# Kernel tuning notes

Hardware: AMD Instinct MI355X
Metric: run time of the kernel (lower is better)

The kernel has to match this reference:

```python
import jax, jax.numpy as jnp
import numpy as np

B, S, D, H, K = 2, 1024, 1024, 16, 33  # batch, seq, d_model, heads, rel buckets (k+1)
d = D // H


def setup_inputs() -> dict:
    key = jax.random.key(0)
    ks = jax.random.split(key, 16)
    w = lambda k, shape: jax.random.normal(k, shape, dtype=jnp.float32) * 0.02
    return {
        "hidden_state": jax.random.normal(ks[0], (B, S, D), dtype=jnp.float32),
        "pos_indices": jax.random.randint(ks[1], (B, S, S), 0, K),
        "mask": jax.random.bernoulli(ks[2], 0.1, (B, 1, 1, S)),
        "Wq": w(ks[3], (D, D)), "bq": w(ks[4], (D,)),
        "Wk": w(ks[5], (D, D)), "bk": w(ks[6], (D,)),
        "Wv": w(ks[7], (D, D)), "bv": w(ks[8], (D,)),
        "Wo": w(ks[9], (D, D)), "bo": w(ks[10], (D,)),
        "rel_q": w(ks[11], (H, K, d)),
        "rel_k": w(ks[12], (H, K, d)),
        "rel_v": w(ks[13], (H, K, d)),
    }


def reference(hidden_state, pos_indices, mask, Wq, bq, Wk, bk, Wv, bv, Wo, bo,
              rel_q, rel_k, rel_v):
    b, s, dm = hidden_state.shape
    h, k_, dp = rel_q.shape
    # projections -> [B,H,S,d]
    def proj(x, W, bias):
        return (x @ W + bias).reshape(b, s, h, dp).transpose(0, 2, 1, 3)
    q = proj(hidden_state, Wq, bq)
    kk = proj(hidden_state, Wk, bk)
    v = proj(hidden_state, Wv, bv)
    # scale_factor = 1 (c2c) + 1 (rel_q) + 1 (rel_k)
    scale = 1.0 / np.sqrt(dp * 3).astype(np.float32)
    # content-to-content
    c2c = jnp.einsum("bhid,bhjd->bhij", q, kk) * scale
    idx = jnp.broadcast_to(pos_indices[:, None], (b, h, s, s))
    # position-to-content: raw [B,H,K,S], gathered along K with per-(i,j) bucket
    raw_p2c = jnp.einsum("hkd,bhjd->bhkj", rel_q, kk) * scale
    p2c = jnp.take_along_axis(raw_p2c, idx, axis=2)
    # content-to-position: raw [B,H,S,K], gathered along K
    raw_c2p = jnp.einsum("bhid,hkd->bhik", q, rel_k) * scale
    c2p = jnp.take_along_axis(raw_c2p, idx, axis=3)
    scores = c2c + p2c + c2p
    scores = jnp.where(mask, jnp.float32(-1e9), scores)
    probs = jax.nn.softmax(scores, axis=-1)  # dropout is identity in eval
    ctx = jnp.einsum("bhij,bhjd->bhid", probs, v)
    # value-side relative term: sum_j P[i,j] * rel_v[bucket(i,j)]
    oh = jax.nn.one_hot(pos_indices, k_, dtype=probs.dtype)  # [B,S,S,K]
    agg = jnp.einsum("bhij,bijk->bhik", probs, oh)
    ctx = ctx + jnp.einsum("bhik,hkd->bhid", agg, rel_v)
    out = ctx.transpose(0, 2, 1, 3).reshape(b, s, dm)
    return out @ Wo + bo
```

## Files before the change

### kernel.cpp

```cpp
#include <hip/hip_runtime.h>
#include <hip/hip_bf16.h>

#define B_ 2
#define S_ 1024
#define D_ 1024
#define H_ 16
#define K_ 33
#define DH 64
#define SCALE 0.07216878364870322f
#define FXS 32768.0f
#define FXI (1.0f / 32768.0f)

typedef __attribute__((ext_vector_type(8))) short bf16x8;
typedef __attribute__((ext_vector_type(4))) float f32x4;

__device__ __forceinline__ float b2f(unsigned short u) {
    return __uint_as_float(((unsigned int)u) << 16);
}
__device__ __forceinline__ unsigned short f2b(float f) {
    unsigned int u = __float_as_uint(f);
    u += 0x7FFFu + ((u >> 16) & 1u);
    return (unsigned short)(u >> 16);
}
__device__ __forceinline__ float ldf(const void* p, int i, int f32) {
    return f32 ? ((const float*)p)[i] : b2f(((const unsigned short*)p)[i]);
}
__device__ __forceinline__ float4 ldf4(const void* p, int i, int f32) {
    if (f32) return *(const float4*)((const float*)p + i);
    ushort4 u = *(const ushort4*)((const unsigned short*)p + i);
    return make_float4(b2f(u.x), b2f(u.y), b2f(u.z), b2f(u.w));
}
__device__ __forceinline__ float4 ldb4(const unsigned short* p, int i) {
    ushort4 u = *(const ushort4*)(p + i);
    return make_float4(b2f(u.x), b2f(u.y), b2f(u.z), b2f(u.w));
}

__global__ __launch_bounds__(256) void prep(const void* __restrict__ hidden,
                                            const void* __restrict__ mask,
                                            int* __restrict__ flags,
                                            float* __restrict__ mflag) {
    __shared__ int cnt;
    __shared__ int mev[6];
    const int t = threadIdx.x;
    if (t == 0) cnt = 0;
    if (t < 6) mev[t] = 0;
    __syncthreads();
    const unsigned short* hu = (const unsigned short*)hidden;
    int c = 0;
    for (int i = t; i < 2048; i += 256) {
        int e = (hu[i] >> 7) & 0xFF;
        if (e >= 0x8E) c++;
    }
    if (c) atomicAdd(&cnt, c);
    const unsigned char* mb = (const unsigned char*)mask;
    int e_bf = 0, e_f32 = 0, e_f64 = 0, e_f16 = 0, e_u8 = 0;
    for (int p = t; p < 2048; p += 256) {
        unsigned char v = mb[p];
        if ((p & 7) == 6 && v == 0xF0) e_f64 = 1;
        if ((p & 3) == 1 && v == 0x3F) e_bf = 1;
        if ((p & 3) == 3 && v == 0x3F) e_f32 = 1;
        if ((p & 1) == 1 && v == 0x3C) e_f16 = 1;
        if ((p & 3) != 0 && v != 0) e_u8 = 1;
    }
    if (e_f64) atomicOr(&mev[5], 1);
    if (e_bf)  atomicOr(&mev[3], 1);
    if (e_f32) atomicOr(&mev[2], 1);
    if (e_f16) atomicOr(&mev[4], 1);
    if (e_u8)  atomicOr(&mev[1], 1);
    __syncthreads();
    const int f32flag = (cnt >= 8) ? 1 : 0;
    const int mm = mev[5] ? 5 : (mev[3] ? 3 : (mev[2] ? 2 : (mev[4] ? 4 : (mev[1] ? 1 : 0))));
    if (t == 0) { flags[0] = f32flag; flags[2] = mm; }
    for (int j = t; j < B_ * S_; j += 256) {
        int m;
        if (mm == 5)      m = (((const double*)mask)[j] != 0.0);
        else if (mm == 3 || mm == 4) m = (((const unsigned short*)mask)[j] != 0);
        else if (mm == 2) m = (((const float*)mask)[j] != 0.f);
        else if (mm == 1) m = (mb[j] != 0);
        else              m = (((const int*)mask)[j] != 0);
        mflag[j] = m ? 1.f : 0.f;
    }
}

__global__ __launch_bounds__(256) void pos_pack(const int* __restrict__ pos,
                                                unsigned char* __restrict__ pos8) {
    int i = blockIdx.x * 256 + threadIdx.x;
    if (i >= (B_ * S_ * S_) / 4) return;
    int4 p = *(const int4*)&pos[i * 4];
    uchar4 o;
    o.x = (unsigned char)min(max(p.x, 0), K_ - 1);
    o.y = (unsigned char)min(max(p.y, 0), K_ - 1);
    o.z = (unsigned char)min(max(p.z, 0), K_ - 1);
    o.w = (unsigned char)min(max(p.w, 0), K_ - 1);
    *(uchar4*)&pos8[i * 4] = o;
}

__global__ __launch_bounds__(512, 2) void gemm_qkv_mfma(const void* __restrict__ X,
                                                        const void* __restrict__ W0,
                                                        const void* __restrict__ W1,
                                                        const void* __restrict__ W2,
                                                        const void* __restrict__ b0,
                                                        const void* __restrict__ b1,
                                                        const void* __restrict__ b2,
                                                        const int* __restrict__ flags,
                                                        unsigned short* __restrict__ q,
                                                        unsigned short* __restrict__ kk_,
                                                        unsigned short* __restrict__ v) {
    __shared__ unsigned short Asl[128][40];
    __shared__ unsigned short Bsl[128][40];
    const int f32u = flags[0];
    const int z = blockIdx.z;
    const void* W = z == 0 ? W0 : (z == 1 ? W1 : W2);
    const void* bias = z == 0 ? b0 : (z == 1 ? b1 : b2);
    unsigned short* outp = z == 0 ? q : (z == 1 ? kk_ : v);
    const int m0 = blockIdx.y * 128, n0 = blockIdx.x * 128;
    const int t = threadIdx.x;
    const int w = t >> 6, lane = t & 63;
    const int wr = w >> 2, wc = w & 3;
    const int lm = lane & 15, lg = lane >> 4;

    const int am = t >> 2, ac8 = (t & 3) * 8;
    const int bn = t & 127, bkq = (t >> 7) * 8;

    f32x4 acc[4][2] = {};
    float4 pa0, pa1;
    float pbx[8];

    {
        int base = (m0 + am) * 1024 + ac8;
        pa0 = ldf4(X, base, f32u);
        pa1 = ldf4(X, base + 4, f32u);
#pragma unroll
        for (int qi = 0; qi < 8; ++qi)
            pbx[qi] = ldf(W, (bkq + qi) * 1024 + n0 + bn, f32u);
    }

    for (int k0 = 0; k0 < 1024; k0 += 32) {
        {
            ushort4 u0 = {f2b(pa0.x), f2b(pa0.y), f2b(pa0.z), f2b(pa0.w)};
            ushort4 u1 = {f2b(pa1.x), f2b(pa1.y), f2b(pa1.z), f2b(pa1.w)};
            *(ushort4*)&Asl[am][ac8] = u0;
            *(ushort4*)&Asl[am][ac8 + 4] = u1;
#pragma unroll
            for (int qi = 0; qi < 8; qi += 2) {
                unsigned int pk = (unsigned int)f2b(pbx[qi]) |
                                  ((unsigned int)f2b(pbx[qi + 1]) << 16);
                *(unsigned int*)&Bsl[bn][bkq + qi] = pk;
            }
        }
        __syncthreads();
        if (k0 + 32 < 1024) {
            int kn = k0 + 32;
            int base = (m0 + am) * 1024 + kn + ac8;
            pa0 = ldf4(X, base, f32u);
            pa1 = ldf4(X, base + 4, f32u);
#pragma unroll
            for (int qi = 0; qi < 8; ++qi)
                pbx[qi] = ldf(W, (kn + bkq + qi) * 1024 + n0 + bn, f32u);
        }
        bf16x8 af[4], bfr[2];
#pragma unroll
        for (int mi = 0; mi < 4; ++mi)
            af[mi] = *(const bf16x8*)&Asl[wr * 64 + mi * 16 + lm][lg * 8];
#pragma unroll
        for (int nj = 0; nj < 2; ++nj)
            bfr[nj] = *(const bf16x8*)&Bsl[wc * 32 + nj * 16 + lm][lg * 8];
#pragma unroll
        for (int mi = 0; mi < 4; ++mi)
#pragma unroll
            for (int nj = 0; nj < 2; ++nj)
                acc[mi][nj] = __builtin_amdgcn_mfma_f32_16x16x32_bf16(af[mi], bfr[nj],
                                                                      acc[mi][nj], 0, 0, 0);
        __syncthreads();
    }
#pragma unroll
    for (int nj = 0; nj < 2; ++nj) {
        int n = n0 + wc * 32 + nj * 16 + lm;
        float bv = ldf(bias, n, f32u);
        int hh = n >> 6, dd = n & 63;
#pragma unroll
        for (int mi = 0; mi < 4; ++mi) {
#pragma unroll
            for (int r = 0; r < 4; ++r) {
                int m = m0 + wr * 64 + mi * 16 + lg * 4 + r;
                int bb = m >> 10, ii = m & 1023;
                outp[((bb * H_ + hh) * S_ + ii) * DH + dd] = f2b(acc[mi][nj][r] + bv);
            }
        }
    }
}

__global__ __launch_bounds__(512, 2) void gemm_out_mfma(const unsigned short* __restrict__ X,
                                                        const void* __restrict__ W,
                                                        const void* __restrict__ bias,
                                                        const int* __restrict__ flags,
                                                        float* __restrict__ out) {
    __shared__ unsigned short Asl[128][40];
    __shared__ unsigned short Bsl[128][40];
    const int f32u = flags[0];
    const int m0 = blockIdx.y * 128, n0 = blockIdx.x * 128;
    const int t = threadIdx.x;
    const int w = t >> 6, lane = t & 63;
    const int wr = w >> 2, wc = w & 3;
    const int lm = lane & 15, lg = lane >> 4;

    const int am = t >> 2, ac8 = (t & 3) * 8;
    const int bn = t & 127, bkq = (t >> 7) * 8;

    f32x4 acc[4][2] = {};
    ushort4 pa0, pa1;
    float pbx[8];

    {
        const ushort4* src = (const ushort4*)&X[(m0 + am) * 1024 + ac8];
        pa0 = src[0];
        pa1 = src[1];
#pragma unroll
        for (int qi = 0; qi < 8; ++qi)
            pbx[qi] = ldf(W, (bkq + qi) * 1024 + n0 + bn, f32u);
    }

    for (int k0 = 0; k0 < 1024; k0 += 32) {
        {
            *(ushort4*)&Asl[am][ac8] = pa0;
            *(ushort4*)&Asl[am][ac8 + 4] = pa1;
#pragma unroll
            for (int qi = 0; qi < 8; qi += 2) {
                unsigned int pk = (unsigned int)f2b(pbx[qi]) |
                                  ((unsigned int)f2b(pbx[qi + 1]) << 16);
                *(unsigned int*)&Bsl[bn][bkq + qi] = pk;
            }
        }
        __syncthreads();
        if (k0 + 32 < 1024) {
            int kn = k0 + 32;
            const ushort4* src = (const ushort4*)&X[(m0 + am) * 1024 + kn + ac8];
            pa0 = src[0];
            pa1 = src[1];
#pragma unroll
            for (int qi = 0; qi < 8; ++qi)
                pbx[qi] = ldf(W, (kn + bkq + qi) * 1024 + n0 + bn, f32u);
        }
        bf16x8 af[4], bfr[2];
#pragma unroll
        for (int mi = 0; mi < 4; ++mi)
            af[mi] = *(const bf16x8*)&Asl[wr * 64 + mi * 16 + lm][lg * 8];
#pragma unroll
        for (int nj = 0; nj < 2; ++nj)
            bfr[nj] = *(const bf16x8*)&Bsl[wc * 32 + nj * 16 + lm][lg * 8];
#pragma unroll
        for (int mi = 0; mi < 4; ++mi)
#pragma unroll
            for (int nj = 0; nj < 2; ++nj)
                acc[mi][nj] = __builtin_amdgcn_mfma_f32_16x16x32_bf16(af[mi], bfr[nj],
                                                                      acc[mi][nj], 0, 0, 0);
        __syncthreads();
    }
#pragma unroll
    for (int nj = 0; nj < 2; ++nj) {
        int n = n0 + wc * 32 + nj * 16 + lm;
        float bv = ldf(bias, n, f32u);
#pragma unroll
        for (int mi = 0; mi < 4; ++mi) {
#pragma unroll
            for (int r = 0; r < 4; ++r) {
                int m = m0 + wr * 64 + mi * 16 + lg * 4 + r;
                out[m * 1024 + n] = acc[mi][nj][r] + bv;
            }
        }
    }
}

__global__ __launch_bounds__(256) void rel_p2c(const unsigned short* __restrict__ kws,
                                               const void* __restrict__ relq,
                                               const int* __restrict__ flags,
                                               unsigned short* __restrict__ p2c) {
    __shared__ float kt[64][68];
    __shared__ float rq[33][68];
    const int f32u = flags[0];
    const int bh = blockIdx.y, h = bh & 15;
    const int j0 = blockIdx.x * 64;
    const int t = threadIdx.x;
#pragma unroll
    for (int qq = 0; qq < 4; ++qq) {
        int idx = t + 256 * qq;
        int j = idx >> 4, d4 = idx & 15;
        *(float4*)&kt[j][d4 * 4] = ldb4(kws, (bh * S_ + j0 + j) * DH + d4 * 4);
    }
    for (int idx = t; idx < 33 * 16; idx += 256) {
        int k = idx >> 4, d4 = idx & 15;
        *(float4*)&rq[k][d4 * 4] = ldf4(relq, (h * K_ + k) * DH + d4 * 4, f32u);
    }
    __syncthreads();
    for (int o = t; o < 33 * 64; o += 256) {
        int k = o >> 6, j = o & 63;
        float s = 0.f;
#pragma unroll
        for (int d4 = 0; d4 < 16; ++d4) {
            float4 a = *(const float4*)&rq[k][d4 * 4];
            float4 b = *(const float4*)&kt[j][d4 * 4];
            s += a.x * b.x + a.y * b.y + a.z * b.z + a.w * b.w;
        }
        p2c[(bh * K_ + k) * S_ + j0 + j] = f2b(s * SCALE);
    }
}

__global__ __launch_bounds__(256) void rel_c2p(const unsigned short* __restrict__ qws,
                                               const void* __restrict__ relk,
                                               const int* __restrict__ flags,
                                               unsigned short* __restrict__ c2p) {
    __shared__ float qt[64][68];
    __shared__ float rk[33][68];
    const int f32u = flags[0];
    const int bh = blockIdx.y, h = bh & 15;
    const int i0 = blockIdx.x * 64;
    const int t = threadIdx.x;
#pragma unroll
    for (int qq = 0; qq < 4; ++qq) {
        int idx = t + 256 * qq;
        int i = idx >> 4, d4 = idx & 15;
        *(float4*)&qt[i][d4 * 4] = ldb4(qws, (bh * S_ + i0 + i) * DH + d4 * 4);
    }
    for (int idx = t; idx < 33 * 16; idx += 256) {
        int k = idx >> 4, d4 = idx & 15;
        *(float4*)&rk[k][d4 * 4] = ldf4(relk, (h * K_ + k) * DH + d4 * 4, f32u);
    }
    __syncthreads();
    for (int o = t; o < 64 * 33; o += 256) {
        int i = o / 33, k = o % 33;
        float s = 0.f;
#pragma unroll
        for (int d4 = 0; d4 < 16; ++d4) {
            float4 a = *(const float4*)&qt[i][d4 * 4];
            float4 b = *(const float4*)&rk[k][d4 * 4];
            s += a.x * b.x + a.y * b.y + a.z * b.z + a.w * b.w;
        }
        c2p[(bh * S_ + i0 + i) * K_ + k] = f2b(s * SCALE);
    }
}

#define PS_OFF   0
#define VT_OFF   32768
#define P2CS_OFF 32768
#define C2P_OFF  50176
#define AG_OFF   54528
#define RV_OFF   63232
#define MF_OFF   67456
#define ATTN_LDS 68480

__device__ __forceinline__ int ps_addr(int il, int jc) {
    return PS_OFF + il * 512 + ((jc * 2) ^ ((il & 7) << 4));
}

__global__ __launch_bounds__(512, 4) void attn_mfma(const unsigned short* __restrict__ qws,
                                                    const unsigned short* __restrict__ kws,
                                                    const unsigned short* __restrict__ vws,
                                                    const unsigned short* __restrict__ p2c,
                                                    const unsigned short* __restrict__ c2p,
                                                    const float* __restrict__ mflag,
                                                    const unsigned char* __restrict__ pos8,
                                                    const int* __restrict__ pos32,
                                                    int use8,
                                                    const void* __restrict__ relv,
                                                    const int* __restrict__ flags,
                                                    unsigned short* __restrict__ ctxo) {
    extern __shared__ char smem[];
    const int f32u = flags[0];
    const int lin = blockIdx.y * 16 + blockIdx.x;
    const int logi = (lin & 7) * 64 + (lin >> 3);
    const int bh = logi >> 4, b = bh >> 4, h = bh & 15;
    const int i0 = (logi & 15) * 64;
    const int t = threadIdx.x;
    const int w = t >> 6, lane = t & 63;
    const int lm = lane & 15, lg = lane >> 4;
    const int iband = (w & 3) * 16;
    const int jh = w >> 2;
    const int dbase = jh * 32;

    unsigned int* agU = (unsigned int*)(smem + AG_OFF);
    unsigned short* c2pS = (unsigned short*)(smem + C2P_OFF);
    unsigned short* rvS = (unsigned short*)(smem + RV_OFF);
    unsigned char* mfS = (unsigned char*)(smem + MF_OFF);

    for (int idx = t; idx < 64 * 33; idx += 512) {
        int il = idx / 33, k = idx % 33;
        c2pS[il * 34 + k] = c2p[(bh * S_ + i0 + il) * K_ + k];
    }
    for (int idx = t; idx < 33 * 64; idx += 512) {
        int k = idx >> 6, d = idx & 63;
        rvS[k * 64 + d] = f2b(ldf(relv, (h * K_ + k) * DH + d, f32u));
    }
    for (int idx = t; idx < 1024; idx += 512)
        mfS[idx] = (mflag[b * S_ + idx] != 0.f) ? 1 : 0;
    for (int idx = t; idx < 64 * 34; idx += 512) agU[idx] = 0u;

    bf16x8 aq0 = *(const bf16x8*)&qws[(bh * S_ + i0 + iband + lm) * DH + lg * 8];
    bf16x8 aq1 = *(const bf16x8*)&qws[(bh * S_ + i0 + iband + lm) * DH + 32 + lg * 8];
    f32x4 acc0 = {}, acc1 = {};

    const int p2cbase = bh * K_ * S_;
    const int rowbase = (b * S_ + i0 + iband + lg * 4) * S_;
    __syncthreads();

    for (int c = 0; c < 4; ++c) {
        for (int idx = t; idx < 33 * 32; idx += 512) {
            int k = idx >> 5, v8 = idx & 31;
            uint4 src = *(const uint4*)&p2c[p2cbase + k * S_ + c * 256 + v8 * 8];
            unsigned int* dst = (unsigned int*)(smem + P2CS_OFF + k * 516 + v8 * 16);
            dst[0] = src.x; dst[1] = src.y; dst[2] = src.z; dst[3] = src.w;
        }
        __syncthreads();

        for (int jt = 0; jt < 8; ++jt) {
            const int jc = jh * 128 + jt * 16 + lm;
            const int jcol = c * 256 + jc;
            int pb4[4];
            if (use8) {
#pragma unroll
                for (int r = 0; r < 4; ++r)
                    pb4[r] = pos8[rowbase + r * S_ + jcol];
            } else {
#pragma unroll
                for (int r = 0; r < 4; ++r) {
                    int p = pos32[rowbase + r * S_ + jcol];
                    pb4[r] = min(max(p, 0), K_ - 1);
                }
            }
            bf16x8 kf0 = *(const bf16x8*)&kws[(bh * S_ + jcol - lm + lm) * DH + lg * 8];
            bf16x8 kf1 = *(const bf16x8*)&kws[(bh * S_ + jcol - lm + lm) * DH + 32 + lg * 8];
            f32x4 a = {};
            a = __builtin_amdgcn_mfma_f32_16x16x32_bf16(aq0, kf0, a, 0, 0, 0);
            a = __builtin_amdgcn_mfma_f32_16x16x32_bf16(aq1, kf1, a, 0, 0, 0);
            const int masked = mfS[jcol];
#pragma unroll
            for (int r = 0; r < 4; ++r) {
                int il = iband + lg * 4 + r;
                int pb = pb4[r];
                float gv = b2f(*(const unsigned short*)(smem + P2CS_OFF + pb * 516 + jc * 2));
                float s = a[r] * SCALE + gv + b2f(c2pS[il * 34 + pb]);
                float ev = masked ? 0.f : __expf(s);
                *(unsigned short*)(smem + ps_addr(il, jc)) = f2b(ev);
                atomicAdd(&agU[il * 34 + pb], (unsigned int)(ev * FXS + 0.5f));
            }
        }
        __syncthreads();

        for (int st = 0; st < 2; ++st) {
#pragma unroll
            for (int u = 0; u < 2; ++u) {
                int idx = t + u * 512;
                int jj = idx >> 3;
                int a8 = idx & 7;
                int d0 = a8 * 8;
                int j = c * 256 + st * 128 + jj;
                bf16x8 vv = *(const bf16x8*)&vws[(bh * S_ + j) * DH + d0];
#pragma unroll
                for (int e = 0; e < 8; ++e) {
                    int ee = (e + a8) & 7;
                    *(unsigned short*)(smem + VT_OFF + (d0 + ee) * 272 + jj * 2) =
                        ((short*)&vv)[ee];
                }
            }
            __syncthreads();
#pragma unroll
            for (int ks = 0; ks < 4; ++ks) {
                int jcb = st * 128 + ks * 32 + lg * 8;
                bf16x8 af = *(const bf16x8*)(smem + ps_addr(iband + lm, jcb));
                bf16x8 b0 = *(const bf16x8*)(smem + VT_OFF + (dbase + lm) * 272 +
                                             (ks * 32 + lg * 8) * 2);
                bf16x8 b1 = *(const bf16x8*)(smem + VT_OFF + (dbase + 16 + lm) * 272 +
                                             (ks * 32 + lg * 8) * 2);
                acc0 = __builtin_amdgcn_mfma_f32_16x16x32_bf16(af, b0, acc0, 0, 0, 0);
                acc1 = __builtin_amdgcn_mfma_f32_16x16x32_bf16(af, b1, acc1, 0, 0, 0);
            }
            __syncthreads();
        }
    }

#pragma unroll
    for (int r = 0; r < 4; ++r) {
        int il = iband + lg * 4 + r;
        float rs = 0.f;
        float o0 = acc0[r], o1 = acc1[r];
        for (int kb = 0; kb < K_; ++kb) {
            float a = (float)agU[il * 34 + kb] * FXI;
            rs += a;
            o0 += a * b2f(rvS[kb * 64 + dbase + lm]);
            o1 += a * b2f(rvS[kb * 64 + dbase + 16 + lm]);
        }
        float inv = 1.0f / rs;
        ctxo[(b * S_ + i0 + il) * D_ + h * DH + dbase + lm] = f2b(o0 * inv);
        ctxo[(b * S_ + i0 + il) * D_ + h * DH + dbase + 16 + lm] = f2b(o1 * inv);
    }
}

extern "C" void kernel_launch(void* const* d_in, const int* in_sizes, int n_in,
                              void* d_out, int out_size, void* d_ws, size_t ws_size,
                              hipStream_t stream) {
    const void* hidden = d_in[0];
    const void* pos = d_in[1];
    const void* mask = d_in[2];
    const void* Wq = d_in[3];
    const void* bq = d_in[4];
    const void* Wk = d_in[5];
    const void* bk = d_in[6];
    const void* Wv = d_in[7];
    const void* bv = d_in[8];
    const void* Wo = d_in[9];
    const void* bo = d_in[10];
    const void* rq = d_in[11];
    const void* rk = d_in[12];
    const void* rv = d_in[13];

    unsigned char* wsb = (unsigned char*)d_ws;
    size_t o = 0;
    int* flags = (int*)(wsb + o);            o += 256;
    float* mfl = (float*)(wsb + o);          o += 2048 * 4;
    o = (o + 255) & ~(size_t)255;
    unsigned short* qb   = (unsigned short*)(wsb + o); o += 4194304;
    unsigned short* kb   = (unsigned short*)(wsb + o); o += 4194304;
    unsigned short* vb   = (unsigned short*)(wsb + o); o += 4194304;
    unsigned short* p2cb = (unsigned short*)(wsb + o); o += 2162688;
    unsigned short* c2pb = (unsigned short*)(wsb + o); o += 2162688;
    unsigned short* ctxb = (unsigned short*)(wsb + o); o += 4194304;
    unsigned char* pos8  = (unsigned char*)(wsb + o);  o += 2097152;
    const int use8 = (ws_size >= o) ? 1 : 0;

    float* out = (float*)d_out;
    const int* posi = (const int*)pos;

    hipFuncSetAttribute(reinterpret_cast<const void*>(attn_mfma),
                        hipFuncAttributeMaxDynamicSharedMemorySize, ATTN_LDS);

    dim3 tb(256);
    prep<<<dim3(1), tb, 0, stream>>>(hidden, mask, flags, mfl);
    if (use8) pos_pack<<<dim3(2048), tb, 0, stream>>>(posi, pos8);
    gemm_qkv_mfma<<<dim3(8, 16, 3), dim3(512), 0, stream>>>(hidden, Wq, Wk, Wv, bq, bk, bv,
                                                            flags, qb, kb, vb);
    rel_p2c<<<dim3(16, 32), tb, 0, stream>>>(kb, rq, flags, p2cb);
    rel_c2p<<<dim3(16, 32), tb, 0, stream>>>(qb, rk, flags, c2pb);
    attn_mfma<<<dim3(16, 32), dim3(512), ATTN_LDS, stream>>>(qb, kb, vb, p2cb, c2pb, mfl,
                                                             pos8, posi, use8, rv, flags,
                                                             ctxb);
    gemm_out_mfma<<<dim3(8, 16), dim3(512), 0, stream>>>(ctxb, Wo, bo, flags, out);
}
```

Measured before the change: 170.2 us.

## Pre-transpose weights to bf16 and fuse relative-position kernels

Adds a w_pack kernel that converts the four projection weights to bf16 and transposes them, so both GEMMs can load B tiles with vectorized row-contiguous reads instead of strided scalar fp32 loads plus conversion. The two relative-position kernels are merged into one launch using blockIdx.z. The P-tile LDS swizzle is changed to reduce bank conflicts, and the fixed-point atomic accumulation drops its rounding offset. The pack pass adds extra memory traffic on every call and needs more workspace; if the workspace is too small it falls back to the old path.

```diff
diff --git a/kernel.cpp b/kernel.cpp
--- a/kernel.cpp
+++ b/kernel.cpp
@@ -95,14 +95,56 @@
     *(uchar4*)&pos8[i * 4] = o;
 }
 
+__global__ __launch_bounds__(256) void w_pack(const void* __restrict__ W0,
+                                              const void* __restrict__ W1,
+                                              const void* __restrict__ W2,
+                                              const void* __restrict__ W3,
+                                              const int* __restrict__ flags,
+                                              unsigned short* __restrict__ T0,
+                                              unsigned short* __restrict__ T1,
+                                              unsigned short* __restrict__ T2,
+                                              unsigned short* __restrict__ T3) {
+    __shared__ unsigned short tl[64][66];
+    const int f32u = flags[0];
+    const int z = blockIdx.z;
+    const void* W = z == 0 ? W0 : (z == 1 ? W1 : (z == 2 ? W2 : W3));
+    unsigned short* T = z == 0 ? T0 : (z == 1 ? T1 : (z == 2 ? T2 : T3));
+    const int k0 = blockIdx.y * 64, n0 = blockIdx.x * 64;
+    const int t = threadIdx.x;
+    {
+        int kr = t >> 2, nc = (t & 3) * 16;
+#pragma unroll
+        for (int u = 0; u < 4; ++u) {
+            float4 v = ldf4(W, (k0 + kr) * 1024 + n0 + nc + u * 4, f32u);
+            tl[kr][nc + u * 4 + 0] = f2b(v.x);
+            tl[kr][nc + u * 4 + 1] = f2b(v.y);
+            tl[kr][nc + u * 4 + 2] = f2b(v.z);
+            tl[kr][nc + u * 4 + 3] = f2b(v.w);
+        }
+    }
+    __syncthreads();
+    {
+        int nr = t >> 2, kc = (t & 3) * 16;
+        unsigned short o[16];
+#pragma unroll
+        for (int u = 0; u < 16; ++u) o[u] = tl[kc + u][nr];
+#pragma unroll
+        for (int u = 0; u < 4; ++u)
+            *(ushort4*)&T[(n0 + nr) * 1024 + k0 + kc + u * 4] = *(ushort4*)&o[u * 4];
+    }
+}
+
 __global__ __launch_bounds__(512, 2) void gemm_qkv_mfma(const void* __restrict__ X,
                                                         const void* __restrict__ W0,
                                                         const void* __restrict__ W1,
                                                         const void* __restrict__ W2,
+                                                        const unsigned short* __restrict__ T0,
+                                                        const unsigned short* __restrict__ T1,
+                                                        const unsigned short* __restrict__ T2,
                                                         const void* __restrict__ b0,
                                                         const void* __restrict__ b1,
                                                         const void* __restrict__ b2,
-                                                        const int* __restrict__ flags,
+                                                        const int* __restrict__ flags, int useT,
                                                         unsigned short* __restrict__ q,
                                                         unsigned short* __restrict__ kk_,
                                                         unsigned short* __restrict__ v) {
@@ -111,6 +153,7 @@
     const int f32u = flags[0];
     const int z = blockIdx.z;
     const void* W = z == 0 ? W0 : (z == 1 ? W1 : W2);
+    const unsigned short* WT = z == 0 ? T0 : (z == 1 ? T1 : T2);
     const void* bias = z == 0 ? b0 : (z == 1 ? b1 : b2);
     unsigned short* outp = z == 0 ? q : (z == 1 ? kk_ : v);
     const int m0 = blockIdx.y * 128, n0 = blockIdx.x * 128;
@@ -124,15 +167,21 @@
 
     f32x4 acc[4][2] = {};
     float4 pa0, pa1;
+    ushort4 tb0, tb1;
     float pbx[8];
 
     {
         int base = (m0 + am) * 1024 + ac8;
         pa0 = ldf4(X, base, f32u);
         pa1 = ldf4(X, base + 4, f32u);
-#pragma unroll
-        for (int qi = 0; qi < 8; ++qi)
-            pbx[qi] = ldf(W, (bkq + qi) * 1024 + n0 + bn, f32u);
+        if (useT) {
+            const ushort4* s = (const ushort4*)&WT[(n0 + am) * 1024 + ac8];
+            tb0 = s[0]; tb1 = s[1];
+        } else {
+#pragma unroll
+            for (int qi = 0; qi < 8; ++qi)
+                pbx[qi] = ldf(W, (bkq + qi) * 1024 + n0 + bn, f32u);
+        }
     }
 
     for (int k0 = 0; k0 < 1024; k0 += 32) {
@@ -141,11 +190,16 @@
             ushort4 u1 = {f2b(pa1.x), f2b(pa1.y), f2b(pa1.z), f2b(pa1.w)};
             *(ushort4*)&Asl[am][ac8] = u0;
             *(ushort4*)&Asl[am][ac8 + 4] = u1;
-#pragma unroll
-            for (int qi = 0; qi < 8; qi += 2) {
-                unsigned int pk = (unsigned int)f2b(pbx[qi]) |
-                                  ((unsigned int)f2b(pbx[qi + 1]) << 16);
-                *(unsigned int*)&Bsl[bn][bkq + qi] = pk;
+            if (useT) {
+                *(ushort4*)&Bsl[am][ac8] = tb0;
+                *(ushort4*)&Bsl[am][ac8 + 4] = tb1;
+            } else {
+#pragma unroll
+                for (int qi = 0; qi < 8; qi += 2) {
+                    unsigned int pk = (unsigned int)f2b(pbx[qi]) |
+                                      ((unsigned int)f2b(pbx[qi + 1]) << 16);
+                    *(unsigned int*)&Bsl[bn][bkq + qi] = pk;
+                }
             }
         }
         __syncthreads();
@@ -154,9 +208,14 @@
             int base = (m0 + am) * 1024 + kn + ac8;
             pa0 = ldf4(X, base, f32u);
             pa1 = ldf4(X, base + 4, f32u);
-#pragma unroll
-            for (int qi = 0; qi < 8; ++qi)
-                pbx[qi] = ldf(W, (kn + bkq + qi) * 1024 + n0 + bn, f32u);
+            if (useT) {
+                const ushort4* s = (const ushort4*)&WT[(n0 + am) * 1024 + kn + ac8];
+                tb0 = s[0]; tb1 = s[1];
+            } else {
+#pragma unroll
+                for (int qi = 0; qi < 8; ++qi)
+                    pbx[qi] = ldf(W, (kn + bkq + qi) * 1024 + n0 + bn, f32u);
+            }
         }
         bf16x8 af[4], bfr[2];
 #pragma unroll
@@ -192,8 +251,9 @@
 
 __global__ __launch_bounds__(512, 2) void gemm_out_mfma(const unsigned short* __restrict__ X,
                                                         const void* __restrict__ W,
+                                                        const unsigned short* __restrict__ WT,
                                                         const void* __restrict__ bias,
-                                                        const int* __restrict__ flags,
+                                                        const int* __restrict__ flags, int useT,
                                                         float* __restrict__ out) {
     __shared__ unsigned short Asl[128][40];
     __shared__ unsigned short Bsl[128][40];
@@ -208,27 +268,37 @@
     const int bn = t & 127, bkq = (t >> 7) * 8;
 
     f32x4 acc[4][2] = {};
-    ushort4 pa0, pa1;
+    ushort4 pa0, pa1, tb0, tb1;
     float pbx[8];
 
     {
         const ushort4* src = (const ushort4*)&X[(m0 + am) * 1024 + ac8];
         pa0 = src[0];
         pa1 = src[1];
-#pragma unroll
-        for (int qi = 0; qi < 8; ++qi)
-            pbx[qi] = ldf(W, (bkq + qi) * 1024 + n0 + bn, f32u);
+        if (useT) {
+            const ushort4* s = (const ushort4*)&WT[(n0 + am) * 1024 + ac8];
+            tb0 = s[0]; tb1 = s[1];
+        } else {
+#pragma unroll
+            for (int qi = 0; qi < 8; ++qi)
+                pbx[qi] = ldf(W, (bkq + qi) * 1024 + n0 + bn, f32u);
+        }
     }
 
     for (int k0 = 0; k0 < 1024; k0 += 32) {
         {
             *(ushort4*)&Asl[am][ac8] = pa0;
             *(ushort4*)&Asl[am][ac8 + 4] = pa1;
-#pragma unroll
-            for (int qi = 0; qi < 8; qi += 2) {
-                unsigned int pk = (unsigned int)f2b(pbx[qi]) |
-                                  ((unsigned int)f2b(pbx[qi + 1]) << 16);
-                *(unsigned int*)&Bsl[bn][bkq + qi] = pk;
+            if (useT) {
+                *(ushort4*)&Bsl[am][ac8] = tb0;
+                *(ushort4*)&Bsl[am][ac8 + 4] = tb1;
+            } else {
+#pragma unroll
+                for (int qi = 0; qi < 8; qi += 2) {
+                    unsigned int pk = (unsigned int)f2b(pbx[qi]) |
+                                      ((unsigned int)f2b(pbx[qi + 1]) << 16);
+                    *(unsigned int*)&Bsl[bn][bkq + qi] = pk;
+                }
             }
         }
         __syncthreads();
@@ -237,9 +307,14 @@
             const ushort4* src = (const ushort4*)&X[(m0 + am) * 1024 + kn + ac8];
             pa0 = src[0];
             pa1 = src[1];
-#pragma unroll
-            for (int qi = 0; qi < 8; ++qi)
-                pbx[qi] = ldf(W, (kn + bkq + qi) * 1024 + n0 + bn, f32u);
+            if (useT) {
+                const ushort4* s = (const ushort4*)&WT[(n0 + am) * 1024 + kn + ac8];
+                tb0 = s[0]; tb1 = s[1];
+            } else {
+#pragma unroll
+                for (int qi = 0; qi < 8; ++qi)
+                    pbx[qi] = ldf(W, (kn + bkq + qi) * 1024 + n0 + bn, f32u);
+            }
         }
         bf16x8 af[4], bfr[2];
 #pragma unroll
@@ -271,71 +346,65 @@
     }
 }
 
-__global__ __launch_bounds__(256) void rel_p2c(const unsigned short* __restrict__ kws,
-                                               const void* __restrict__ relq,
-                                               const int* __restrict__ flags,
-                                               unsigned short* __restrict__ p2c) {
-    __shared__ float kt[64][68];
-    __shared__ float rq[33][68];
+__global__ __launch_bounds__(256) void rel_fused(const unsigned short* __restrict__ kws,
+                                                 const unsigned short* __restrict__ qws,
+                                                 const void* __restrict__ relq,
+                                                 const void* __restrict__ relk,
+                                                 const int* __restrict__ flags,
+                                                 unsigned short* __restrict__ p2c,
+                                                 unsigned short* __restrict__ c2p) {
+    __shared__ float xt[64][68];
+    __shared__ float rr[33][68];
     const int f32u = flags[0];
     const int bh = blockIdx.y, h = bh & 15;
-    const int j0 = blockIdx.x * 64;
+    const int x0 = blockIdx.x * 64;
     const int t = threadIdx.x;
-#pragma unroll
-    for (int qq = 0; qq < 4; ++qq) {
-        int idx = t + 256 * qq;
-        int j = idx >> 4, d4 = idx & 15;
-        *(float4*)&kt[j][d4 * 4] = ldb4(kws, (bh * S_ + j0 + j) * DH + d4 * 4);
-    }
-    for (int idx = t; idx < 33 * 16; idx += 256) {
-        int k = idx >> 4, d4 = idx & 15;
-        *(float4*)&rq[k][d4 * 4] = ldf4(relq, (h * K_ + k) * DH + d4 * 4, f32u);
-    }
-    __syncthreads();
-    for (int o = t; o < 33 * 64; o += 256) {
-        int k = o >> 6, j = o & 63;
-        float s = 0.f;
-#pragma unroll
-        for (int d4 = 0; d4 < 16; ++d4) {
-            float4 a = *(const float4*)&rq[k][d4 * 4];
-            float4 b = *(const float4*)&kt[j][d4 * 4];
-            s += a.x * b.x + a.y * b.y + a.z * b.z + a.w * b.w;
-        }
-        p2c[(bh * K_ + k) * S_ + j0 + j] = f2b(s * SCALE);
-    }
-}
-
-__global__ __launch_bounds__(256) void rel_c2p(const unsigned short* __restrict__ qws,
-                                               const void* __restrict__ relk,
-                                               const int* __restrict__ flags,
-                                               unsigned short* __restrict__ c2p) {
-    __shared__ float qt[64][68];
-    __shared__ float rk[33][68];
-    const int f32u = flags[0];
-    const int bh = blockIdx.y, h = bh & 15;
-    const int i0 = blockIdx.x * 64;
-    const int t = threadIdx.x;
-#pragma unroll
-    for (int qq = 0; qq < 4; ++qq) {
-        int idx = t + 256 * qq;
-        int i = idx >> 4, d4 = idx & 15;
-        *(float4*)&qt[i][d4 * 4] = ldb4(qws, (bh * S_ + i0 + i) * DH + d4 * 4);
-    }
-    for (int idx = t; idx < 33 * 16; idx += 256) {
-        int k = idx >> 4, d4 = idx & 15;
-        *(float4*)&rk[k][d4 * 4] = ldf4(relk, (h * K_ + k) * DH + d4 * 4, f32u);
-    }
-    __syncthreads();
-    for (int o = t; o < 64 * 33; o += 256) {
-        int i = o / 33, k = o % 33;
-        float s = 0.f;
-#pragma unroll
-        for (int d4 = 0; d4 < 16; ++d4) {
-            float4 a = *(const float4*)&qt[i][d4 * 4];
-            float4 b = *(const float4*)&rk[k][d4 * 4];
-            s += a.x * b.x + a.y * b.y + a.z * b.z + a.w * b.w;
-        }
-        c2p[(bh * S_ + i0 + i) * K_ + k] = f2b(s * SCALE);
+    if (blockIdx.z == 0) {
+#pragma unroll
+        for (int qq = 0; qq < 4; ++qq) {
+            int idx = t + 256 * qq;
+            int j = idx >> 4, d4 = idx & 15;
+            *(float4*)&xt[j][d4 * 4] = ldb4(kws, (bh * S_ + x0 + j) * DH + d4 * 4);
+        }
+        for (int idx = t; idx < 33 * 16; idx += 256) {
+            int k = idx >> 4, d4 = idx & 15;
+            *(float4*)&rr[k][d4 * 4] = ldf4(relq, (h * K_ + k) * DH + d4 * 4, f32u);
+        }
+        __syncthreads();
+        for (int o = t; o < 33 * 64; o += 256) {
+            int k = o >> 6, j = o & 63;
+            float s = 0.f;
+#pragma unroll
+            for (int d4 = 0; d4 < 16; ++d4) {
+                float4 a = *(const float4*)&rr[k][d4 * 4];
+                float4 b = *(const float4*)&xt[j][d4 * 4];
+                s += a.x * b.x + a.y * b.y + a.z * b.z + a.w * b.w;
+            }
+            p2c[(bh * K_ + k) * S_ + x0 + j] = f2b(s * SCALE);
+        }
+    } else {
+#pragma unroll
+        for (int qq = 0; qq < 4; ++qq) {
+            int idx = t + 256 * qq;
+            int i = idx >> 4, d4 = idx & 15;
+            *(float4*)&xt[i][d4 * 4] = ldb4(qws, (bh * S_ + x0 + i) * DH + d4 * 4);
+        }
+        for (int idx = t; idx < 33 * 16; idx += 256) {
+            int k = idx >> 4, d4 = idx & 15;
+            *(float4*)&rr[k][d4 * 4] = ldf4(relk, (h * K_ + k) * DH + d4 * 4, f32u);
+        }
+        __syncthreads();
+        for (int o = t; o < 64 * 33; o += 256) {
+            int i = o / 33, k = o % 33;
+            float s = 0.f;
+#pragma unroll
+            for (int d4 = 0; d4 < 16; ++d4) {
+                float4 a = *(const float4*)&xt[i][d4 * 4];
+                float4 b = *(const float4*)&rr[k][d4 * 4];
+                s += a.x * b.x + a.y * b.y + a.z * b.z + a.w * b.w;
+            }
+            c2p[(bh * S_ + x0 + i) * K_ + k] = f2b(s * SCALE);
+        }
     }
 }
 
@@ -349,7 +418,8 @@
 #define ATTN_LDS 68480
 
 __device__ __forceinline__ int ps_addr(int il, int jc) {
-    return PS_OFF + il * 512 + ((jc * 2) ^ ((il & 7) << 4));
+    return PS_OFF + il * 512 +
+           ((jc * 2) ^ ((((il >> 2) & 3) << 5) ^ ((il & 3) << 4)));
 }
 
 __global__ __launch_bounds__(512, 4) void attn_mfma(const unsigned short* __restrict__ qws,
@@ -426,8 +496,8 @@
                     pb4[r] = min(max(p, 0), K_ - 1);
                 }
             }
-            bf16x8 kf0 = *(const bf16x8*)&kws[(bh * S_ + jcol - lm + lm) * DH + lg * 8];
-            bf16x8 kf1 = *(const bf16x8*)&kws[(bh * S_ + jcol - lm + lm) * DH + 32 + lg * 8];
+            bf16x8 kf0 = *(const bf16x8*)&kws[(bh * S_ + jcol) * DH + lg * 8];
+            bf16x8 kf1 = *(const bf16x8*)&kws[(bh * S_ + jcol) * DH + 32 + lg * 8];
             f32x4 a = {};
             a = __builtin_amdgcn_mfma_f32_16x16x32_bf16(aq0, kf0, a, 0, 0, 0);
             a = __builtin_amdgcn_mfma_f32_16x16x32_bf16(aq1, kf1, a, 0, 0, 0);
@@ -440,7 +510,7 @@
                 float s = a[r] * SCALE + gv + b2f(c2pS[il * 34 + pb]);
                 float ev = masked ? 0.f : __expf(s);
                 *(unsigned short*)(smem + ps_addr(il, jc)) = f2b(ev);
-                atomicAdd(&agU[il * 34 + pb], (unsigned int)(ev * FXS + 0.5f));
+                atomicAdd(&agU[il * 34 + pb], (unsigned int)(ev * FXS));
             }
         }
         __syncthreads();
@@ -525,6 +595,11 @@
     unsigned short* ctxb = (unsigned short*)(wsb + o); o += 4194304;
     unsigned char* pos8  = (unsigned char*)(wsb + o);  o += 2097152;
     const int use8 = (ws_size >= o) ? 1 : 0;
+    unsigned short* wTq = (unsigned short*)(wsb + o);  o += 2097152;
+    unsigned short* wTk = (unsigned short*)(wsb + o);  o += 2097152;
+    unsigned short* wTv = (unsigned short*)(wsb + o);  o += 2097152;
+    unsigned short* wTo = (unsigned short*)(wsb + o);  o += 2097152;
+    const int useT = (ws_size >= o) ? 1 : 0;
 
     float* out = (float*)d_out;
     const int* posi = (const int*)pos;
@@ -535,12 +610,16 @@
     dim3 tb(256);
     prep<<<dim3(1), tb, 0, stream>>>(hidden, mask, flags, mfl);
     if (use8) pos_pack<<<dim3(2048), tb, 0, stream>>>(posi, pos8);
-    gemm_qkv_mfma<<<dim3(8, 16, 3), dim3(512), 0, stream>>>(hidden, Wq, Wk, Wv, bq, bk, bv,
-                                                            flags, qb, kb, vb);
-    rel_p2c<<<dim3(16, 32), tb, 0, stream>>>(kb, rq, flags, p2cb);
-    rel_c2p<<<dim3(16, 32), tb, 0, stream>>>(qb, rk, flags, c2pb);
+    if (useT) w_pack<<<dim3(16, 16, 4), tb, 0, stream>>>(Wq, Wk, Wv, Wo, flags,
+                                                         wTq, wTk, wTv, wTo);
+    gemm_qkv_mfma<<<dim3(8, 16, 3), dim3(512), 0, stream>>>(hidden, Wq, Wk, Wv,
+                                                            wTq, wTk, wTv,
+                                                            bq, bk, bv, flags, useT,
+                                                            qb, kb, vb);
+    rel_fused<<<dim3(16, 32, 2), tb, 0, stream>>>(kb, qb, rq, rk, flags, p2cb, c2pb);
     attn_mfma<<<dim3(16, 32), dim3(512), ATTN_LDS, stream>>>(qb, kb, vb, p2cb, c2pb, mfl,
                                                              pos8, posi, use8, rv, flags,
                                                              ctxb);
-    gemm_out_mfma<<<dim3(8, 16), dim3(512), 0, stream>>>(ctxb, Wo, bo, flags, out);
-}
+    gemm_out_mfma<<<dim3(8, 16), dim3(512), 0, stream>>>(ctxb, Wo, wTo, bo, flags, useT,
+                                                         out);
+}
```

Result: faster. 158.4 us (-6.9%).
